# Kernel tuning notes

Hardware: AMD Instinct MI355X
Metric: run time of the kernel (lower is better)

## Reference

```python
import jax, jax.numpy as jnp
import numpy as np

B, S, H, NH, DH, I, C, P = 4, 1024, 1280, 20, 64, 5120, 13, 8
LN_EPS = 1e-5


def setup_inputs() -> dict:
    key = jax.random.key(0)
    ks = jax.random.split(key, 20)
    n = lambda k, shp, s=0.02: (jax.random.normal(k, shp, jnp.float32) * s)
    return {
        "hidden_states": jax.random.normal(ks[0], (B, S, H), jnp.float32),
        "attention_mask": jnp.ones((B, S), jnp.float32),
        "Wq": n(ks[1], (H, H)), "bq": jnp.zeros((H,), jnp.float32),
        "Wk": n(ks[2], (H, H)), "bk": jnp.zeros((H,), jnp.float32),
        "Wv": n(ks[3], (H, H)), "bv": jnp.zeros((H,), jnp.float32),
        "W_ct1": n(ks[4], (P, C), 0.3), "b_ct1": jnp.zeros((P,), jnp.float32),
        "W_ct2": n(ks[5], (P, C), 0.3), "b_ct2": jnp.zeros((P,), jnp.float32),
        "M": n(ks[6], (C, C), 0.5),
        "bias_scale": jnp.full((1,), 0.5, jnp.float32),
        "W_ptm": n(ks[7], (P, H)), "b_ptm": jnp.zeros((P,), jnp.float32),
        "ln_g": jnp.ones((H,), jnp.float32), "ln_b": jnp.zeros((H,), jnp.float32),
        "Wf1": n(ks[8], (I, H)), "bf1": jnp.zeros((I,), jnp.float32),
        "Wf2": n(ks[9], (H, I)), "bf2": jnp.zeros((H,), jnp.float32),
    }


def reference(hidden_states, attention_mask, Wq, bq, Wk, bk, Wv, bv,
              W_ct1, b_ct1, W_ct2, b_ct2, M, bias_scale, W_ptm, b_ptm,
              ln_g, ln_b, Wf1, bf1, Wf2, bf2):
    h = hidden_states
    # crosstalk bilinear projection: (P,C) @ (C,P) -> (P,P)
    out1 = (M.T @ W_ct1.T + b_ct1).T          # (P, C)
    out2 = M @ W_ct2.T + b_ct2                # (C, P)
    R = out1 @ out2                           # (P, P)
    # ptm_predictor (Linear H->P) + softmax
    ptm = jax.nn.softmax(h @ W_ptm.T + b_ptm, axis=-1)            # (B,S,P)
    Bb = jnp.tanh(jnp.einsum('blc,cd,bmd->blm', ptm, R, ptm)) * bias_scale  # (B,S,S)
    # manual multi-head attention
    q = (h @ Wq.T + bq).reshape(B, S, NH, DH).transpose(0, 2, 1, 3)
    k = (h @ Wk.T + bk).reshape(B, S, NH, DH).transpose(0, 2, 1, 3)
    v = (h @ Wv.T + bv).reshape(B, S, NH, DH).transpose(0, 2, 1, 3)
    scores = jnp.einsum('bhld,bhmd->bhlm', q, k) / np.float32(np.sqrt(DH))
    scores = scores + Bb[:, None]
    scores = scores + (1.0 - attention_mask)[:, None, None, :] * jnp.finfo(h.dtype).min
    probs = jax.nn.softmax(scores, axis=-1)
    ctx = jnp.einsum('bhlm,bhmd->bhld', probs, v)
    ctx = ctx.transpose(0, 2, 1, 3).reshape(B, S, H)
    # residual + LayerNorm
    x = h + ctx
    mu = jnp.mean(x, -1, keepdims=True)
    var = jnp.var(x, -1, keepdims=True)
    x = (x - mu) * jax.lax.rsqrt(var + LN_EPS) * ln_g + ln_b
    # FFN with exact GELU, residual
    ff = jax.nn.gelu(x @ Wf1.T + bf1, approximate=False) @ Wf2.T + bf2
    return x + ff
```

## Files before the change

kernel.cpp:

```cpp
#include <hip/hip_runtime.h>
#include <math.h>

typedef _Float16 f16;
typedef _Float16 f16x2 __attribute__((ext_vector_type(2)));
typedef _Float16 f16x8 __attribute__((ext_vector_type(8)));
typedef _Float16 f16x4 __attribute__((ext_vector_type(4)));
typedef float f32x4 __attribute__((ext_vector_type(4)));

#define B_ 4
#define S_ 1024
#define H_ 1280
#define NH_ 20
#define DH_ 64
#define I_ 5120
#define C_ 13
#define P_ 8
#define LOG2E 1.44269504088896f

__device__ __forceinline__ void store_val(float* p, float v) { *p = v; }
__device__ __forceinline__ void store_val(f16* p, float v) { *p = (f16)v; }

__device__ __forceinline__ float fast_gelu(float x) {
    float ax = 0.70710678118654752f * fabsf(x);
    float t = __builtin_amdgcn_rcpf(1.0f + 0.3275911f * ax);
    float p = t * (0.254829592f + t * (-0.284496736f + t * (1.421413741f
              + t * (-1.453152027f + t * 1.061405429f))));
    float e = __builtin_exp2f(-(LOG2E) * ax * ax);
    float er = 1.0f - p * e;
    float cdf = 0.5f + 0.5f * (x >= 0.0f ? er : -er);
    return x * cdf;
}

__device__ __forceinline__ float fast_tanh(float x) {
    x = fminf(fmaxf(x, -20.0f), 20.0f);
    float e = __builtin_exp2f(x * (2.0f * LOG2E));
    return (e - 1.0f) * __builtin_amdgcn_rcpf(e + 1.0f);
}

__global__ __launch_bounds__(256) void cvt5_kernel(
    const float* __restrict__ s0, f16* __restrict__ d0, int n0,
    const float* __restrict__ s1, f16* __restrict__ d1, int n1,
    const float* __restrict__ s2, f16* __restrict__ d2, int n2,
    const float* __restrict__ s3, f16* __restrict__ d3, int n3,
    const float* __restrict__ s4, f16* __restrict__ d4, int n4) {
    int seg = blockIdx.y;
    const float* src = (seg == 0) ? s0 : (seg == 1) ? s1 : (seg == 2) ? s2
                     : (seg == 3) ? s3 : s4;
    f16* dst = (seg == 0) ? d0 : (seg == 1) ? d1 : (seg == 2) ? d2
             : (seg == 3) ? d3 : d4;
    int n = (seg == 0) ? n0 : (seg == 1) ? n1 : (seg == 2) ? n2
          : (seg == 3) ? n3 : n4;
    int i = blockIdx.x * 256 + threadIdx.x;
    if (i < n) {
        f32x4 v = ((const f32x4*)src)[i];
        f16x4 o;
#pragma unroll
        for (int e = 0; e < 4; e++) o[e] = (f16)v[e];
        ((f16x4*)dst)[i] = o;
    }
}

__global__ __launch_bounds__(256) void ptm_kernel(const float* __restrict__ hin,
                                                  const float* __restrict__ Wptm,
                                                  const float* __restrict__ bptm,
                                                  const float* __restrict__ Mg,
                                                  const float* __restrict__ W1,
                                                  const float* __restrict__ b1,
                                                  const float* __restrict__ W2,
                                                  const float* __restrict__ b2,
                                                  float* __restrict__ ptm,
                                                  float* __restrict__ tg,
                                                  f16* __restrict__ hin16) {
    __shared__ float o1[P_][C_];
    __shared__ float o2[C_][P_];
    __shared__ float R[P_ * P_];
    int t = threadIdx.x;
    if (t < P_ * C_) {
        int p = t / C_, c = t % C_;
        float s = b1[p];
        for (int k = 0; k < C_; k++) s += Mg[k * C_ + c] * W1[p * C_ + k];
        o1[p][c] = s;
        int c2 = t / P_, p2 = t % P_;
        float s2 = b2[p2];
        for (int k = 0; k < C_; k++) s2 += Mg[c2 * C_ + k] * W2[p2 * C_ + k];
        o2[c2][p2] = s2;
    }
    __syncthreads();
    if (t < P_ * P_) {
        int p = t >> 3, q = t & 7;
        float s = 0.f;
        for (int c = 0; c < C_; c++) s += o1[p][c] * o2[c][q];
        R[t] = s;
    }
    __syncthreads();

    int wv = t >> 6, lane = t & 63;
    int row = blockIdx.x * 4 + wv;
    const float* hrow = hin + (size_t)row * H_;
    f16* hrow16 = hin16 + (size_t)row * H_;
    float acc[P_] = {};
    for (int i = 0; i < H_ / 64; i++) {
        int k = lane + 64 * i;
        float hv = hrow[k];
        hrow16[k] = (f16)hv;
#pragma unroll
        for (int p = 0; p < P_; p++) acc[p] += hv * Wptm[p * H_ + k];
    }
#pragma unroll
    for (int p = 0; p < P_; p++) {
#pragma unroll
        for (int o = 32; o >= 1; o >>= 1) acc[p] += __shfl_xor(acc[p], o);
        acc[p] += bptm[p];
    }
    float mx = acc[0];
#pragma unroll
    for (int p = 1; p < P_; p++) mx = fmaxf(mx, acc[p]);
    float sum = 0.f;
#pragma unroll
    for (int p = 0; p < P_; p++) { acc[p] = expf(acc[p] - mx); sum += acc[p]; }
    float rinv = 1.f / sum;
#pragma unroll
    for (int p = 0; p < P_; p++) acc[p] *= rinv;
    float tv[P_];
#pragma unroll
    for (int d = 0; d < P_; d++) {
        float s = 0.f;
#pragma unroll
        for (int c = 0; c < P_; c++) s += acc[c] * R[c * P_ + d];
        tv[d] = s;
    }
    if (lane == 0) {
#pragma unroll
        for (int p = 0; p < P_; p++) {
            ptm[(size_t)row * P_ + p] = acc[p];
            tg[(size_t)row * P_ + p]  = tv[p];
        }
    }
}

__global__ __launch_bounds__(256) void bias_kernel(const float* __restrict__ tg,
                                                   const float* __restrict__ ptm,
                                                   const float* __restrict__ mask,
                                                   const float* __restrict__ bscale_p,
                                                   f16* __restrict__ bb) {
    const int bl = blockIdx.x;
    const int b = bl >> 10;
    const int t = threadIdx.x;
    __shared__ float tl[P_];
    if (t < P_) tl[t] = tg[(size_t)bl * P_ + t];
    __syncthreads();
    const float bscale = bscale_p[0];
    float t0 = tl[0], t1 = tl[1], t2 = tl[2], t3 = tl[3];
    float t4 = tl[4], t5 = tl[5], t6 = tl[6], t7 = tl[7];
#pragma unroll
    for (int i = 0; i < 4; i++) {
        int m = t + 256 * i;
        const float* pm = ptm + ((size_t)b * S_ + m) * P_;
        float4 p0 = *(const float4*)pm;
        float4 p1 = *(const float4*)(pm + 4);
        float d = t0 * p0.x + t1 * p0.y + t2 * p0.z + t3 * p0.w
                + t4 * p1.x + t5 * p1.y + t6 * p1.z + t7 * p1.w;
        float v = (fast_tanh(d) * bscale + (1.0f - mask[(size_t)b * S_ + m]) * (-30000.0f)) * LOG2E;
        bb[(size_t)bl * S_ + m] = (f16)v;
    }
}

template <int MODE, typename YT>
__device__ __forceinline__ void gemm_body(const f16* __restrict__ X,
                                          const f16* __restrict__ W,
                                          const float* __restrict__ bias,
                                          YT* __restrict__ Y,
                                          const f16* __restrict__ res,
                                          int Ndim, int Kdim, int kbeg, int kend,
                                          int m0, int n0, f16* sA, f16* sB) {
    const int t = threadIdx.x;
    const int lane = t & 63, w = t >> 6;
    const int wr = w >> 1, wc = w & 1;
    const int lr = lane & 15, kq = lane >> 4;

    f32x4 acc[4][4] = {};

    int s_row[4], s_gc[4];
#pragma unroll
    for (int inst = 0; inst < 4; inst++) {
        int ci = t + 256 * inst;
        s_row[inst] = ci >> 3;
        s_gc[inst] = (ci & 7) ^ (s_row[inst] & 7);
    }

    for (int k0 = kbeg; k0 < kend; k0 += 64) {
        __syncthreads();
#pragma unroll
        for (int inst = 0; inst < 4; inst++) {
            int ci = t + 256 * inst;
            __builtin_amdgcn_global_load_lds(
                (const unsigned*)(X + (size_t)(m0 + s_row[inst]) * Kdim + k0 + s_gc[inst] * 8),
                (unsigned*)(sA + ci * 8), 16, 0, 0);
        }
#pragma unroll
        for (int inst = 0; inst < 4; inst++) {
            int ci = t + 256 * inst;
            __builtin_amdgcn_global_load_lds(
                (const unsigned*)(W + (size_t)(n0 + s_row[inst]) * Kdim + k0 + s_gc[inst] * 8),
                (unsigned*)(sB + ci * 8), 16, 0, 0);
        }
        __syncthreads();
#pragma unroll
        for (int ks = 0; ks < 2; ks++) {
            f16x8 af[4], bf[4];
#pragma unroll
            for (int i = 0; i < 4; i++) {
                int row = wr * 64 + i * 16 + lr;
                int cl = (ks * 4 + kq) ^ (row & 7);
                af[i] = *(const f16x8*)(sA + row * 64 + cl * 8);
            }
#pragma unroll
            for (int j = 0; j < 4; j++) {
                int row = wc * 64 + j * 16 + lr;
                int cl = (ks * 4 + kq) ^ (row & 7);
                bf[j] = *(const f16x8*)(sB + row * 64 + cl * 8);
            }
#pragma unroll
            for (int i = 0; i < 4; i++)
#pragma unroll
                for (int j = 0; j < 4; j++)
                    acc[i][j] = __builtin_amdgcn_mfma_f32_16x16x32_f16(af[i], bf[j], acc[i][j], 0, 0, 0);
        }
    }
#pragma unroll
    for (int j = 0; j < 4; j++) {
        int col = n0 + wc * 64 + j * 16 + lr;
        float bcol = (MODE == 3) ? 0.f : bias[col];
#pragma unroll
        for (int i = 0; i < 4; i++) {
#pragma unroll
            for (int rr = 0; rr < 4; rr++) {
                int row = m0 + wr * 64 + i * 16 + kq * 4 + rr;
                float v = acc[i][j][rr] + bcol;
                if (MODE == 1) v = fast_gelu(v);
                store_val(&Y[(size_t)row * Ndim + col], v);
            }
        }
    }
}

template <int MODE, typename YT>
__global__ __launch_bounds__(256, 2) void gemm128(const f16* __restrict__ X,
                                                  const f16* __restrict__ W,
                                                  const float* __restrict__ bias,
                                                  YT* __restrict__ Y,
                                                  const f16* __restrict__ res,
                                                  int Ndim, int Kdim) {
    __shared__ f16 sA[128 * 64];
    __shared__ f16 sB[128 * 64];
    gemm_body<MODE, YT>(X, W, bias, Y, res, Ndim, Kdim, 0, Kdim,
                        blockIdx.x * 128, blockIdx.y * 128, sA, sB);
}

__global__ __launch_bounds__(256, 2) void gemm_qkv(const f16* __restrict__ X,
                                                   const f16* __restrict__ Wq,
                                                   const f16* __restrict__ Wk,
                                                   const f16* __restrict__ Wv,
                                                   const float* __restrict__ bq,
                                                   const float* __restrict__ bk,
                                                   const float* __restrict__ bv,
                                                   f16* __restrict__ qb,
                                                   f16* __restrict__ kb,
                                                   f16* __restrict__ vb) {
    __shared__ f16 sA[128 * 64];
    __shared__ f16 sB[128 * 64];
    const int g = blockIdx.y / 10, nt = blockIdx.y % 10;
    const f16* W = (g == 0) ? Wq : (g == 1) ? Wk : Wv;
    const float* bias = (g == 0) ? bq : (g == 1) ? bk : bv;
    f16* Y = (g == 0) ? qb : (g == 1) ? kb : vb;
    gemm_body<0, f16>(X, W, bias, Y, nullptr, H_, H_, 0, H_,
                      blockIdx.x * 128, nt * 128, sA, sB);
}

__global__ __launch_bounds__(512, 2) void gemm256_sk(const f16* __restrict__ X,
                                                     const f16* __restrict__ W,
                                                     float* __restrict__ p0,
                                                     float* __restrict__ p1,
                                                     float* __restrict__ p2,
                                                     int Ndim, int Kdim) {
    __shared__ f16 sA[2 * 16384];
    __shared__ f16 sB[2 * 16384];
    const int z = blockIdx.z;
    float* __restrict__ Y = (z == 0) ? p0 : (z == 1) ? p1 : p2;
    const int kbeg = z * 1728;
    const int kend = (z == 2) ? Kdim : kbeg + 1728;
    const int NT = (kend - kbeg) >> 6;
    const int m0 = blockIdx.x * 256, n0 = blockIdx.y * 256;

    const int t = threadIdx.x;
    const int lane = t & 63, w = t >> 6;
    const int wr = w >> 2, wc = w & 3;
    const int lr = lane & 15, kq = lane >> 4;

    const int rh0 = t >> 3;
    const int gc0 = (t & 7) ^ (rh0 & 7);
    const f16* Asrc = X + (size_t)(m0 + rh0) * Kdim + kbeg + gc0 * 8;
    const f16* Bsrc = W + (size_t)(n0 + rh0) * Kdim + kbeg + gc0 * 8;

    f32x4 acc[8][4] = {};

#define STG_A(kt_) do { f16* d_ = sA + ((kt_) & 1) * 16384 + t * 8;            \
        const f16* s_ = Asrc + (size_t)(kt_) * 64;                             \
        __builtin_amdgcn_global_load_lds((const unsigned*)s_, (unsigned*)d_, 16, 0, 0); \
        __builtin_amdgcn_global_load_lds((const unsigned*)(s_ + (size_t)64 * Kdim),  (unsigned*)(d_ + 4096), 16, 0, 0);  \
        __builtin_amdgcn_global_load_lds((const unsigned*)(s_ + (size_t)128 * Kdim), (unsigned*)(d_ + 8192), 16, 0, 0);  \
        __builtin_amdgcn_global_load_lds((const unsigned*)(s_ + (size_t)192 * Kdim), (unsigned*)(d_ + 12288), 16, 0, 0); \
    } while (0)
#define STG_B(kt_) do { f16* d_ = sB + ((kt_) & 1) * 16384 + t * 8;            \
        const f16* s_ = Bsrc + (size_t)(kt_) * 64;                             \
        __builtin_amdgcn_global_load_lds((const unsigned*)s_, (unsigned*)d_, 16, 0, 0); \
        __builtin_amdgcn_global_load_lds((const unsigned*)(s_ + (size_t)64 * Kdim),  (unsigned*)(d_ + 4096), 16, 0, 0);  \
        __builtin_amdgcn_global_load_lds((const unsigned*)(s_ + (size_t)128 * Kdim), (unsigned*)(d_ + 8192), 16, 0, 0);  \
        __builtin_amdgcn_global_load_lds((const unsigned*)(s_ + (size_t)192 * Kdim), (unsigned*)(d_ + 12288), 16, 0, 0); \
    } while (0)

    STG_A(0); STG_B(0);
    if (NT > 1) {
        STG_A(1); STG_B(1);
        asm volatile("s_waitcnt vmcnt(8)");
    } else {
        asm volatile("s_waitcnt vmcnt(0)");
    }
    __builtin_amdgcn_s_barrier();

    for (int kt = 0; kt < NT; ++kt) {
        const int p = kt & 1;
        const f16* cA = sA + p * 16384;
        const f16* cB = sB + p * 16384;
        f16x8 a[4][2], b0[2][2], b1[2][2];

#pragma unroll
        for (int i = 0; i < 4; ++i) {
            const int r = wr * 128 + (i + 4) * 16 + lr;
#pragma unroll
            for (int ks = 0; ks < 2; ++ks)
                a[i][ks] = *(const f16x8*)(cA + r * 64 + (((ks * 4 + kq) ^ (r & 7)) * 8));
        }
#pragma unroll
        for (int j = 0; j < 2; ++j) {
            const int rb = wc * 64 + j * 16 + lr;
#pragma unroll
            for (int ks = 0; ks < 2; ++ks)
                b0[j][ks] = *(const f16x8*)(cB + rb * 64 + (((ks * 4 + kq) ^ (rb & 7)) * 8));
        }
        __builtin_amdgcn_s_barrier();
        __builtin_amdgcn_s_setprio(1);
#pragma unroll
        for (int ks = 0; ks < 2; ++ks)
#pragma unroll
            for (int i = 0; i < 4; ++i)
#pragma unroll
                for (int j = 0; j < 2; ++j)
                    acc[i + 4][j] = __builtin_amdgcn_mfma_f32_16x16x32_f16(
                        a[i][ks], b0[j][ks], acc[i + 4][j], 0, 0, 0);
        __builtin_amdgcn_s_setprio(0);
        __builtin_amdgcn_s_barrier();

#pragma unroll
        for (int j = 0; j < 2; ++j) {
            const int rb = wc * 64 + (j + 2) * 16 + lr;
#pragma unroll
            for (int ks = 0; ks < 2; ++ks)
                b1[j][ks] = *(const f16x8*)(cB + rb * 64 + (((ks * 4 + kq) ^ (rb & 7)) * 8));
        }
        __builtin_amdgcn_s_barrier();
        __builtin_amdgcn_s_setprio(1);
#pragma unroll
        for (int ks = 0; ks < 2; ++ks)
#pragma unroll
            for (int i = 0; i < 4; ++i)
#pragma unroll
                for (int j = 0; j < 2; ++j)
                    acc[i + 4][j + 2] = __builtin_amdgcn_mfma_f32_16x16x32_f16(
                        a[i][ks], b1[j][ks], acc[i + 4][j + 2], 0, 0, 0);
        __builtin_amdgcn_s_setprio(0);
        __builtin_amdgcn_s_barrier();

#pragma unroll
        for (int i = 0; i < 4; ++i) {
            const int r = wr * 128 + i * 16 + lr;
#pragma unroll
            for (int ks = 0; ks < 2; ++ks)
                a[i][ks] = *(const f16x8*)(cA + r * 64 + (((ks * 4 + kq) ^ (r & 7)) * 8));
        }
        if (kt + 2 < NT) STG_B(kt + 2);
        __builtin_amdgcn_s_barrier();
        __builtin_amdgcn_s_setprio(1);
#pragma unroll
        for (int ks = 0; ks < 2; ++ks)
#pragma unroll
            for (int i = 0; i < 4; ++i)
#pragma unroll
                for (int j = 0; j < 2; ++j)
                    acc[i][j] = __builtin_amdgcn_mfma_f32_16x16x32_f16(
                        a[i][ks], b0[j][ks], acc[i][j], 0, 0, 0);
        __builtin_amdgcn_s_setprio(0);
        __builtin_amdgcn_s_barrier();

        if (kt + 2 < NT) STG_A(kt + 2);
        __builtin_amdgcn_s_setprio(1);
#pragma unroll
        for (int ks = 0; ks < 2; ++ks)
#pragma unroll
            for (int i = 0; i < 4; ++i)
#pragma unroll
                for (int j = 0; j < 2; ++j)
                    acc[i][j + 2] = __builtin_amdgcn_mfma_f32_16x16x32_f16(
                        a[i][ks], b1[j][ks], acc[i][j + 2], 0, 0, 0);
        __builtin_amdgcn_s_setprio(0);
        if (kt + 2 < NT) asm volatile("s_waitcnt vmcnt(8)");
        else             asm volatile("s_waitcnt vmcnt(0)");
        __builtin_amdgcn_s_barrier();
    }
#undef STG_A
#undef STG_B

#pragma unroll
    for (int j = 0; j < 4; ++j) {
        const int col = n0 + wc * 64 + j * 16 + lr;
#pragma unroll
        for (int i = 0; i < 8; ++i) {
#pragma unroll
            for (int rr = 0; rr < 4; ++rr) {
                const int row = m0 + wr * 128 + i * 16 + kq * 4 + rr;
                Y[(size_t)row * Ndim + col] = acc[i][j][rr];
            }
        }
    }
}

__global__ __launch_bounds__(256) void reduce3_kernel(const float* __restrict__ p0,
                                                      const float* __restrict__ p1,
                                                      const float* __restrict__ p2,
                                                      const float* __restrict__ bias,
                                                      const f16* __restrict__ res,
                                                      float* __restrict__ out) {
    int i = blockIdx.x * 256 + threadIdx.x;
    int col = (i * 4) % H_;
    f32x4 a = ((const f32x4*)p0)[i];
    f32x4 b = ((const f32x4*)p1)[i];
    f32x4 c = ((const f32x4*)p2)[i];
    f32x4 bc = *(const f32x4*)(bias + col);
    f16x4 r = ((const f16x4*)res)[i];
    f32x4 o;
#pragma unroll
    for (int e = 0; e < 4; e++) o[e] = a[e] + b[e] + c[e] + bc[e] + (float)r[e];
    ((f32x4*)out)[i] = o;
}

__global__ __launch_bounds__(256) void attn_kernel(const f16* __restrict__ q,
                                                   const f16* __restrict__ k,
                                                   const f16* __restrict__ v,
                                                   const f16* __restrict__ bb,
                                                   const float* __restrict__ hin,
                                                   float* __restrict__ xpre) {
    __shared__ f16 sK[64 * 72];
    __shared__ f16 sVT[64 * 72];
    __shared__ f16 sP[64 * 72];

    const int t = threadIdx.x;
    const int w = t >> 6, lane = t & 63;
    const int lr = lane & 15, kq = lane >> 4;
    const int gid = blockIdx.x + 16 * (blockIdx.y + 20 * blockIdx.z);
    const int wk = (gid & 7) * 160 + (gid >> 3);
    const int l0 = (wk & 15) * 64;
    const int hb = wk >> 4;
    const int h = hb % 20, b = hb / 20;
    const size_t base = (size_t)b * S_ * H_ + (size_t)h * DH_;

    const int kr0 = t >> 3, kc8 = (t & 7) * 8;
    const int vr2 = (t >> 3) * 2, vc8 = (t & 7) * 8;
    const int vmsw = vr2 ^ vc8;
    const int br = t >> 2, bc16 = (t & 3) * 16;
    const f16* bbrow0 = bb + ((size_t)b * S_ + l0 + br) * S_;

    f16x8 kA0 = *(const f16x8*)&k[base + (size_t)kr0 * H_ + kc8];
    f16x8 kA1 = *(const f16x8*)&k[base + (size_t)(kr0 + 32) * H_ + kc8];
    f16x8 vA0 = *(const f16x8*)&v[base + (size_t)vr2 * H_ + vc8];
    f16x8 vA1 = *(const f16x8*)&v[base + (size_t)(vr2 + 1) * H_ + vc8];
    f16x8 bA0 = *(const f16x8*)(bbrow0 + bc16);
    f16x8 bA1 = *(const f16x8*)(bbrow0 + bc16 + 8);

    f16x8 afq[2];
#pragma unroll
    for (int ks = 0; ks < 2; ks++) {
        f16x8 qv = *(const f16x8*)&q[base + (size_t)(l0 + w * 16 + lr) * H_ + ks * 32 + kq * 8];
#pragma unroll
        for (int e = 0; e < 8; e++) qv[e] = (f16)((float)qv[e] * (0.125f * LOG2E));
        afq[ks] = qv;
    }

    f32x4 acc_o[4] = {};
    float lstate[4] = {};

    for (int mt = 0; mt < 16; mt++) {
        __syncthreads();
        *(f16x8*)&sK[kr0 * 72 + kc8] = kA0;
        *(f16x8*)&sK[(kr0 + 32) * 72 + kc8] = kA1;
#pragma unroll
        for (int e = 0; e < 8; e++) {
            f16x2 pk = {vA0[e], vA1[e]};
            *(f16x2*)&sVT[(vc8 + e) * 72 + vmsw] = pk;
        }
        *(f16x8*)&sP[br * 72 + bc16] = bA0;
        *(f16x8*)&sP[br * 72 + bc16 + 8] = bA1;
        const int m1 = ((mt + 1) & 15) * 64;
        f16x8 kB0 = *(const f16x8*)&k[base + (size_t)(m1 + kr0) * H_ + kc8];
        f16x8 kB1 = *(const f16x8*)&k[base + (size_t)(m1 + kr0 + 32) * H_ + kc8];
        f16x8 vB0 = *(const f16x8*)&v[base + (size_t)(m1 + vr2) * H_ + vc8];
        f16x8 vB1 = *(const f16x8*)&v[base + (size_t)(m1 + vr2 + 1) * H_ + vc8];
        f16x8 bB0 = *(const f16x8*)(bbrow0 + m1 + bc16);
        f16x8 bB1 = *(const f16x8*)(bbrow0 + m1 + bc16 + 8);
        __syncthreads();

        f32x4 sacc[4] = {};
        __builtin_amdgcn_s_setprio(1);
#pragma unroll
        for (int ks = 0; ks < 2; ks++)
#pragma unroll
            for (int j = 0; j < 4; j++) {
                f16x8 bk = *(const f16x8*)&sK[(j * 16 + lr) * 72 + ks * 32 + kq * 8];
                sacc[j] = __builtin_amdgcn_mfma_f32_16x16x32_f16(afq[ks], bk, sacc[j], 0, 0, 0);
            }
        __builtin_amdgcn_s_setprio(0);

#pragma unroll
        for (int j = 0; j < 4; j++)
#pragma unroll
            for (int rr = 0; rr < 4; rr++) {
                const int sp_addr = (w * 16 + kq * 4 + rr) * 72 + j * 16 + lr;
                float p = __builtin_exp2f(sacc[j][rr] + (float)sP[sp_addr]);
                lstate[rr] += p;
                sP[sp_addr] = (f16)p;
            }

        f16x8 ap[2];
        ap[0] = *(const f16x8*)&sP[(w * 16 + lr) * 72 + kq * 8];
        ap[1] = *(const f16x8*)&sP[(w * 16 + lr) * 72 + 32 + kq * 8];
        __builtin_amdgcn_s_setprio(1);
#pragma unroll
        for (int ks = 0; ks < 2; ks++)
#pragma unroll
            for (int j2 = 0; j2 < 4; j2++) {
                int d = j2 * 16 + lr;
                int s_ = (d >> 3) & 7;
                f16x8 bv = *(const f16x8*)&sVT[d * 72 + 8 * (((ks << 2) + kq) ^ s_)];
                acc_o[j2] = __builtin_amdgcn_mfma_f32_16x16x32_f16(ap[ks], bv, acc_o[j2], 0, 0, 0);
            }
        __builtin_amdgcn_s_setprio(0);
        kA0 = kB0; kA1 = kB1; vA0 = vB0; vA1 = vB1; bA0 = bB0; bA1 = bB1;
    }

#pragma unroll
    for (int rr = 0; rr < 4; rr++) {
#pragma unroll
        for (int off = 8; off >= 1; off >>= 1) lstate[rr] += __shfl_xor(lstate[rr], off);
    }

#pragma unroll
    for (int rr = 0; rr < 4; rr++) {
        float linv = 1.0f / lstate[rr];
        int tok = l0 + w * 16 + kq * 4 + rr;
        size_t obase = base + (size_t)tok * H_;
#pragma unroll
        for (int j2 = 0; j2 < 4; j2++) {
            int d = j2 * 16 + lr;
            xpre[obase + d] = hin[obase + d] + acc_o[j2][rr] * linv;
        }
    }
}

__global__ __launch_bounds__(256) void ln_kernel(const float* __restrict__ xpre,
                                                 const float* __restrict__ g,
                                                 const float* __restrict__ bb,
                                                 f16* __restrict__ xln) {
    int row = blockIdx.x, t = threadIdx.x;
    const float* xr = xpre + (size_t)row * H_;
    float xv[5], s1 = 0.f, s2 = 0.f;
#pragma unroll
    for (int i = 0; i < 5; i++) {
        float v = xr[t + 256 * i];
        xv[i] = v; s1 += v; s2 += v * v;
    }
#pragma unroll
    for (int o = 32; o >= 1; o >>= 1) { s1 += __shfl_xor(s1, o); s2 += __shfl_xor(s2, o); }
    __shared__ float r1[4], r2[4];
    int wv = t >> 6, lane = t & 63;
    if (lane == 0) { r1[wv] = s1; r2[wv] = s2; }
    __syncthreads();
    float m1 = (r1[0] + r1[1] + r1[2] + r1[3]) * (1.0f / H_);
    float m2 = (r2[0] + r2[1] + r2[2] + r2[3]) * (1.0f / H_);
    float rstd = rsqrtf(m2 - m1 * m1 + 1e-5f);
#pragma unroll
    for (int i = 0; i < 5; i++) {
        int c = t + 256 * i;
        float v = (xv[i] - m1) * rstd * g[c] + bb[c];
        xln[(size_t)row * H_ + c] = (f16)v;
    }
}

extern "C" void kernel_launch(void* const* d_in, const int* in_sizes, int n_in,
                              void* d_out, int out_size, void* d_ws, size_t ws_size,
                              hipStream_t stream) {
    (void)in_sizes; (void)n_in; (void)out_size; (void)ws_size;
    const float* hin  = (const float*)d_in[0];
    const float* mask = (const float*)d_in[1];
    const float* Wq = (const float*)d_in[2];  const float* bq = (const float*)d_in[3];
    const float* Wk = (const float*)d_in[4];  const float* bk = (const float*)d_in[5];
    const float* Wv = (const float*)d_in[6];  const float* bv = (const float*)d_in[7];
    const float* Wct1 = (const float*)d_in[8];  const float* bct1 = (const float*)d_in[9];
    const float* Wct2 = (const float*)d_in[10]; const float* bct2 = (const float*)d_in[11];
    const float* Mg = (const float*)d_in[12];   const float* bscale = (const float*)d_in[13];
    const float* Wptm = (const float*)d_in[14]; const float* bptm = (const float*)d_in[15];
    const float* lng = (const float*)d_in[16];  const float* lnb = (const float*)d_in[17];
    const float* Wf1 = (const float*)d_in[18];  const float* bf1 = (const float*)d_in[19];
    const float* Wf2 = (const float*)d_in[20];  const float* bf2 = (const float*)d_in[21];

    char* ws = (char*)d_ws;
    const size_t SZ_PT  = (size_t)B_ * S_ * P_ * 4;
    const size_t SZ_H16 = (size_t)B_ * S_ * H_ * 2;
    const size_t SZ_H32 = (size_t)B_ * S_ * H_ * 4;
    const size_t SZ_WH  = (size_t)H_ * H_ * 2;
    const size_t SZ_WI  = (size_t)I_ * H_ * 2;
    float* ptm  = (float*)(ws + 256);
    float* tg   = (float*)(ws + 256 + SZ_PT);
    char* A0    = ws + 256 + 2 * SZ_PT;
    f16* hin16  = (f16*)(A0);
    f16* qb     = (f16*)(A0 + SZ_H16);
    f16* kb     = (f16*)(A0 + 2 * SZ_H16);
    f16* vb     = (f16*)(A0 + 3 * SZ_H16);
    float* xpre = (float*)(A0 + 4 * SZ_H16);
    f16* xln    = (f16*)(A0 + 4 * SZ_H16 + SZ_H32);
    f16* bbias  = (f16*)(A0 + 5 * SZ_H16 + SZ_H32);
    char* WA    = A0 + 5 * SZ_H16 + SZ_H32 + (size_t)B_ * S_ * S_ * 2;
    f16* Wq16   = (f16*)(WA);
    f16* Wk16   = (f16*)(WA + SZ_WH);
    f16* Wv16   = (f16*)(WA + 2 * SZ_WH);
    f16* Wf116  = (f16*)(WA + 3 * SZ_WH);
    f16* Wf216  = (f16*)(WA + 3 * SZ_WH + SZ_WI);
    f16* g1     = (f16*)(A0);
    float* pbuf = (float*)(WA + 3 * SZ_WH + 2 * SZ_WI);

    const int NW4 = (H_ * H_) / 4, NI4 = (I_ * H_) / 4;
    cvt5_kernel<<<dim3((NI4 + 255) / 256, 5), 256, 0, stream>>>(
        Wq, Wq16, NW4, Wk, Wk16, NW4, Wv, Wv16, NW4,
        Wf1, Wf116, NI4, Wf2, Wf216, NI4);

    ptm_kernel<<<S_ * B_ / 4, 256, 0, stream>>>(hin, Wptm, bptm,
                                                Mg, Wct1, bct1, Wct2, bct2, ptm, tg, hin16);
    bias_kernel<<<B_ * S_, 256, 0, stream>>>(tg, ptm, mask, bscale, bbias);
    gemm_qkv<<<dim3(32, 30), 256, 0, stream>>>(hin16, Wq16, Wk16, Wv16, bq, bk, bv, qb, kb, vb);
    attn_kernel<<<dim3(S_ / 64, NH_, B_), 256, 0, stream>>>(qb, kb, vb, bbias, hin, xpre);
    ln_kernel<<<B_ * S_, 256, 0, stream>>>(xpre, lng, lnb, xln);
    gemm128<1, f16><<<dim3(32, I_ / 128), 256, 0, stream>>>(xln, Wf116, bf1, g1, nullptr, I_, H_);
    gemm256_sk<<<dim3(16, H_ / 256, 3), 512, 0, stream>>>(
        g1, Wf216, pbuf, pbuf + (size_t)B_ * S_ * H_, xpre, H_, I_);
    reduce3_kernel<<<(B_ * S_ * H_) / 4 / 256, 256, 0, stream>>>(
        pbuf, pbuf + (size_t)B_ * S_ * H_, xpre, bf2, xln, (float*)d_out);
}
```

Before: 454.4 us.

## Fuse QKV projection into one 256-tile GEMM with interleaved QKV output

```diff
diff --git a/kernel.cpp b/kernel.cpp
--- a/kernel.cpp
+++ b/kernel.cpp
@@ -15,6 +15,7 @@
 #define I_ 5120
 #define C_ 13
 #define P_ 8
+#define QS_ 3840
 #define LOG2E 1.44269504088896f
 
 __device__ __forceinline__ void store_val(float* p, float v) { *p = v; }
@@ -257,41 +258,14 @@
                         blockIdx.x * 128, blockIdx.y * 128, sA, sB);
 }
 
-__global__ __launch_bounds__(256, 2) void gemm_qkv(const f16* __restrict__ X,
-                                                   const f16* __restrict__ Wq,
-                                                   const f16* __restrict__ Wk,
-                                                   const f16* __restrict__ Wv,
-                                                   const float* __restrict__ bq,
-                                                   const float* __restrict__ bk,
-                                                   const float* __restrict__ bv,
-                                                   f16* __restrict__ qb,
-                                                   f16* __restrict__ kb,
-                                                   f16* __restrict__ vb) {
-    __shared__ f16 sA[128 * 64];
-    __shared__ f16 sB[128 * 64];
-    const int g = blockIdx.y / 10, nt = blockIdx.y % 10;
-    const f16* W = (g == 0) ? Wq : (g == 1) ? Wk : Wv;
-    const float* bias = (g == 0) ? bq : (g == 1) ? bk : bv;
-    f16* Y = (g == 0) ? qb : (g == 1) ? kb : vb;
-    gemm_body<0, f16>(X, W, bias, Y, nullptr, H_, H_, 0, H_,
-                      blockIdx.x * 128, nt * 128, sA, sB);
-}
-
-__global__ __launch_bounds__(512, 2) void gemm256_sk(const f16* __restrict__ X,
-                                                     const f16* __restrict__ W,
-                                                     float* __restrict__ p0,
-                                                     float* __restrict__ p1,
-                                                     float* __restrict__ p2,
-                                                     int Ndim, int Kdim) {
-    __shared__ f16 sA[2 * 16384];
-    __shared__ f16 sB[2 * 16384];
-    const int z = blockIdx.z;
-    float* __restrict__ Y = (z == 0) ? p0 : (z == 1) ? p1 : p2;
-    const int kbeg = z * 1728;
-    const int kend = (z == 2) ? Kdim : kbeg + 1728;
+template <int MODE, typename YT>
+__device__ __forceinline__ void g256_body(const f16* __restrict__ X,
+                                          const f16* __restrict__ W,
+                                          const float* __restrict__ bias,
+                                          YT* __restrict__ Y,
+                                          int Ndim, int Kdim, int kbeg, int kend,
+                                          int m0, int n0, f16* sA, f16* sB) {
     const int NT = (kend - kbeg) >> 6;
-    const int m0 = blockIdx.x * 256, n0 = blockIdx.y * 256;
-
     const int t = threadIdx.x;
     const int lane = t & 63, w = t >> 6;
     const int wr = w >> 2, wc = w & 3;
@@ -423,15 +397,48 @@
 #pragma unroll
     for (int j = 0; j < 4; ++j) {
         const int col = n0 + wc * 64 + j * 16 + lr;
+        const float bcol = (MODE == 3) ? 0.f : bias[col];
 #pragma unroll
         for (int i = 0; i < 8; ++i) {
 #pragma unroll
             for (int rr = 0; rr < 4; ++rr) {
                 const int row = m0 + wr * 128 + i * 16 + kq * 4 + rr;
-                Y[(size_t)row * Ndim + col] = acc[i][j][rr];
+                float v = acc[i][j][rr] + bcol;
+                store_val(&Y[(size_t)row * Ndim + col], v);
             }
         }
     }
+}
+
+__global__ __launch_bounds__(512, 2) void gemm256_sk(const f16* __restrict__ X,
+                                                     const f16* __restrict__ W,
+                                                     float* __restrict__ p0,
+                                                     float* __restrict__ p1,
+                                                     float* __restrict__ p2,
+                                                     int Ndim, int Kdim) {
+    __shared__ f16 sA[2 * 16384];
+    __shared__ f16 sB[2 * 16384];
+    const int z = blockIdx.z;
+    float* __restrict__ Y = (z == 0) ? p0 : (z == 1) ? p1 : p2;
+    const int kbeg = z * 1728;
+    const int kend = (z == 2) ? Kdim : kbeg + 1728;
+    g256_body<3, float>(X, W, nullptr, Y, Ndim, Kdim, kbeg, kend,
+                        blockIdx.x * 256, blockIdx.y * 256, sA, sB);
+}
+
+__global__ __launch_bounds__(512, 2) void gemm256_qkv(const f16* __restrict__ X,
+                                                      const f16* __restrict__ Wqkv,
+                                                      const float* __restrict__ bq,
+                                                      const float* __restrict__ bk,
+                                                      const float* __restrict__ bv,
+                                                      f16* __restrict__ Y) {
+    __shared__ f16 sA[2 * 16384];
+    __shared__ f16 sB[2 * 16384];
+    const int nt = blockIdx.y;
+    const int g = nt / 5;
+    const float* bsel = (g == 0) ? bq : (g == 1) ? bk : bv;
+    g256_body<0, f16>(X, Wqkv, bsel - (size_t)g * 1280, Y, QS_, H_, 0, H_,
+                      blockIdx.x * 256, nt * 256, sA, sB);
 }
 
 __global__ __launch_bounds__(256) void reduce3_kernel(const float* __restrict__ p0,
@@ -453,9 +460,7 @@
     ((f32x4*)out)[i] = o;
 }
 
-__global__ __launch_bounds__(256) void attn_kernel(const f16* __restrict__ q,
-                                                   const f16* __restrict__ k,
-                                                   const f16* __restrict__ v,
+__global__ __launch_bounds__(256) void attn_kernel(const f16* __restrict__ qkv,
                                                    const f16* __restrict__ bb,
                                                    const float* __restrict__ hin,
                                                    float* __restrict__ xpre) {
@@ -471,7 +476,10 @@
     const int l0 = (wk & 15) * 64;
     const int hb = wk >> 4;
     const int h = hb % 20, b = hb / 20;
-    const size_t base = (size_t)b * S_ * H_ + (size_t)h * DH_;
+    const size_t base  = (size_t)b * S_ * H_ + (size_t)h * DH_;
+    const size_t baseq = (size_t)b * S_ * QS_ + (size_t)h * DH_;
+    const size_t kbase = baseq + 1280;
+    const size_t vbase = baseq + 2560;
 
     const int kr0 = t >> 3, kc8 = (t & 7) * 8;
     const int vr2 = (t >> 3) * 2, vc8 = (t & 7) * 8;
@@ -479,17 +487,17 @@
     const int br = t >> 2, bc16 = (t & 3) * 16;
     const f16* bbrow0 = bb + ((size_t)b * S_ + l0 + br) * S_;
 
-    f16x8 kA0 = *(const f16x8*)&k[base + (size_t)kr0 * H_ + kc8];
-    f16x8 kA1 = *(const f16x8*)&k[base + (size_t)(kr0 + 32) * H_ + kc8];
-    f16x8 vA0 = *(const f16x8*)&v[base + (size_t)vr2 * H_ + vc8];
-    f16x8 vA1 = *(const f16x8*)&v[base + (size_t)(vr2 + 1) * H_ + vc8];
+    f16x8 kA0 = *(const f16x8*)&qkv[kbase + (size_t)kr0 * QS_ + kc8];
+    f16x8 kA1 = *(const f16x8*)&qkv[kbase + (size_t)(kr0 + 32) * QS_ + kc8];
+    f16x8 vA0 = *(const f16x8*)&qkv[vbase + (size_t)vr2 * QS_ + vc8];
+    f16x8 vA1 = *(const f16x8*)&qkv[vbase + (size_t)(vr2 + 1) * QS_ + vc8];
     f16x8 bA0 = *(const f16x8*)(bbrow0 + bc16);
     f16x8 bA1 = *(const f16x8*)(bbrow0 + bc16 + 8);
 
     f16x8 afq[2];
 #pragma unroll
     for (int ks = 0; ks < 2; ks++) {
-        f16x8 qv = *(const f16x8*)&q[base + (size_t)(l0 + w * 16 + lr) * H_ + ks * 32 + kq * 8];
+        f16x8 qv = *(const f16x8*)&qkv[baseq + (size_t)(l0 + w * 16 + lr) * QS_ + ks * 32 + kq * 8];
 #pragma unroll
         for (int e = 0; e < 8; e++) qv[e] = (f16)((float)qv[e] * (0.125f * LOG2E));
         afq[ks] = qv;
@@ -510,10 +518,10 @@
         *(f16x8*)&sP[br * 72 + bc16] = bA0;
         *(f16x8*)&sP[br * 72 + bc16 + 8] = bA1;
         const int m1 = ((mt + 1) & 15) * 64;
-        f16x8 kB0 = *(const f16x8*)&k[base + (size_t)(m1 + kr0) * H_ + kc8];
-        f16x8 kB1 = *(const f16x8*)&k[base + (size_t)(m1 + kr0 + 32) * H_ + kc8];
-        f16x8 vB0 = *(const f16x8*)&v[base + (size_t)(m1 + vr2) * H_ + vc8];
-        f16x8 vB1 = *(const f16x8*)&v[base + (size_t)(m1 + vr2 + 1) * H_ + vc8];
+        f16x8 kB0 = *(const f16x8*)&qkv[kbase + (size_t)(m1 + kr0) * QS_ + kc8];
+        f16x8 kB1 = *(const f16x8*)&qkv[kbase + (size_t)(m1 + kr0 + 32) * QS_ + kc8];
+        f16x8 vB0 = *(const f16x8*)&qkv[vbase + (size_t)(m1 + vr2) * QS_ + vc8];
+        f16x8 vB1 = *(const f16x8*)&qkv[vbase + (size_t)(m1 + vr2 + 1) * QS_ + vc8];
         f16x8 bB0 = *(const f16x8*)(bbrow0 + m1 + bc16);
         f16x8 bB1 = *(const f16x8*)(bbrow0 + m1 + bc16 + 8);
         __syncthreads();
@@ -631,9 +639,7 @@
     float* tg   = (float*)(ws + 256 + SZ_PT);
     char* A0    = ws + 256 + 2 * SZ_PT;
     f16* hin16  = (f16*)(A0);
-    f16* qb     = (f16*)(A0 + SZ_H16);
-    f16* kb     = (f16*)(A0 + 2 * SZ_H16);
-    f16* vb     = (f16*)(A0 + 3 * SZ_H16);
+    f16* qkvb   = (f16*)(A0 + SZ_H16);
     float* xpre = (float*)(A0 + 4 * SZ_H16);
     f16* xln    = (f16*)(A0 + 4 * SZ_H16 + SZ_H32);
     f16* bbias  = (f16*)(A0 + 5 * SZ_H16 + SZ_H32);
@@ -654,8 +660,8 @@
     ptm_kernel<<<S_ * B_ / 4, 256, 0, stream>>>(hin, Wptm, bptm,
                                                 Mg, Wct1, bct1, Wct2, bct2, ptm, tg, hin16);
     bias_kernel<<<B_ * S_, 256, 0, stream>>>(tg, ptm, mask, bscale, bbias);
-    gemm_qkv<<<dim3(32, 30), 256, 0, stream>>>(hin16, Wq16, Wk16, Wv16, bq, bk, bv, qb, kb, vb);
-    attn_kernel<<<dim3(S_ / 64, NH_, B_), 256, 0, stream>>>(qb, kb, vb, bbias, hin, xpre);
+    gemm256_qkv<<<dim3(16, 15), 512, 0, stream>>>(hin16, Wq16, bq, bk, bv, qkvb);
+    attn_kernel<<<dim3(S_ / 64, NH_, B_), 256, 0, stream>>>(qkvb, bbias, hin, xpre);
     ln_kernel<<<B_ * S_, 256, 0, stream>>>(xpre, lng, lnb, xln);
     gemm128<1, f16><<<dim3(32, I_ / 128), 256, 0, stream>>>(xln, Wf116, bf1, g1, nullptr, I_, H_);
     gemm256_sk<<<dim3(16, H_ / 256, 3), 512, 0, stream>>>(
```

New measurement: 455.5 us. Within noise of the previous version (+0.2%).
